# Kernel tuning notes

Measured on AMD Instinct MI355X. Metric: run time of the kernel, lower is better.

The kernel has to match this reference:

```python
import jax, jax.numpy as jnp
import numpy as np

N = 40000
K = 16
NUM_CLASSES = 8
BN_EPS = 1e-5


def _mlp(h, W1, b1, g, bt, m, v, W2, b2):
    # Linear -> ReLU -> BatchNorm1d (eval mode, running stats) -> Linear
    h = jax.nn.relu(h @ W1 + b1)
    h = (h - m) / jnp.sqrt(v + BN_EPS) * g + bt
    return h @ W2 + b2


def _normals(pos, nbr):
    # cross product of first two neighbor offsets, normalized; fallback [0,0,1]
    v1 = pos[nbr[:, 0]] - pos
    v2 = pos[nbr[:, 1]] - pos
    n = jnp.cross(v1, v2)
    nrm = jnp.linalg.norm(n, axis=-1, keepdims=True)
    unit = n / jnp.maximum(nrm, 1e-12)
    up = jnp.array([0.0, 0.0, 1.0], dtype=pos.dtype)
    return jnp.where(nrm > 0, unit, up)


def _pointnet_conv(x, pos, nbr_all, W1, b1, g, bt, m, v, W2, b2):
    # PyG PointNetConv: msg = local_nn(cat[x_j, pos_j - pos_i]); max-aggregate
    xj = x[nbr_all]                        # [N, K+1, F]
    rel = pos[nbr_all] - pos[:, None, :]   # [N, K+1, 3]
    msg = _mlp(jnp.concatenate([xj, rel], axis=-1), W1, b1, g, bt, m, v, W2, b2)
    return msg.max(axis=1)


def setup_inputs():
    key = jax.random.key(0)
    ks = jax.random.split(key, 32)

    def lin_w(k, fi, fo):
        return (jax.random.normal(k, (fi, fo), jnp.float32) / np.sqrt(fi)).astype(jnp.float32)

    def vec(k, d, scale=0.01):
        return scale * jax.random.normal(k, (d,), jnp.float32)

    return {
        "pos": jax.random.normal(ks[0], (N, 3), jnp.float32),
        "neighbor_idx": jax.random.randint(ks[1], (N, K), 0, N),
        # local_features: Linear(9,64), ReLU, BN(64), Linear(64,128)
        "W1": lin_w(ks[2], 9, 64), "b1": vec(ks[3], 64),
        "g1": 1.0 + 0.1 * jax.random.normal(ks[4], (64,), jnp.float32),
        "bt1": vec(ks[5], 64), "m1": vec(ks[6], 64, 0.1),
        "v1": jax.random.uniform(ks[7], (64,), jnp.float32, minval=0.5, maxval=1.5),
        "W2": lin_w(ks[8], 64, 128), "b2": vec(ks[9], 128),
        # roof_features: Linear(131,128), ReLU, BN(128), Linear(128,256)
        "W3": lin_w(ks[10], 131, 128), "b3": vec(ks[11], 128),
        "g2": 1.0 + 0.1 * jax.random.normal(ks[12], (128,), jnp.float32),
        "bt2": vec(ks[13], 128), "m2": vec(ks[14], 128, 0.1),
        "v2": jax.random.uniform(ks[15], (128,), jnp.float32, minval=0.5, maxval=1.5),
        "W4": lin_w(ks[16], 128, 256), "b4": vec(ks[17], 256),
        # classifier: Linear(256, num_classes)
        "Wc": lin_w(ks[18], 256, NUM_CLASSES), "bc": vec(ks[19], NUM_CLASSES),
    }


def reference(pos, neighbor_idx, W1, b1, g1, bt1, m1, v1, W2, b2,
              W3, b3, g2, bt2, m2, v2, W4, b4, Wc, bc):
    x = pos  # data.x is used as both features and coordinates
    normals = _normals(pos, neighbor_idx)
    x = jnp.concatenate([x, normals], axis=1)  # [N, 6]
    # PointNetConv adds self-loops by default
    self_idx = jnp.arange(pos.shape[0], dtype=neighbor_idx.dtype)[:, None]
    nbr_all = jnp.concatenate([neighbor_idx, self_idx], axis=1)  # [N, K+1]
    x = jax.nn.relu(_pointnet_conv(x, pos, nbr_all, W1, b1, g1, bt1, m1, v1, W2, b2))
    x = jax.nn.relu(_pointnet_conv(x, pos, nbr_all, W3, b3, g2, bt2, m2, v2, W4, b4))
    logits = x @ Wc + bc
    return jax.nn.log_softmax(logits, axis=-1)
```

## Files before the change

kernel.cpp:

```cpp
#include <hip/hip_runtime.h>
#include <math.h>

#define NPTS 40000
#define KNBR 16
#define BN_EPS 1e-5f

typedef __attribute__((ext_vector_type(8))) short v8s;
typedef __attribute__((ext_vector_type(4))) float f32x4;

__device__ __forceinline__ unsigned short f2bf(float f) {
    union { float f; unsigned int u; } c; c.f = f;
    unsigned int u = c.u + 0x7fffu + ((c.u >> 16) & 1u);
    return (unsigned short)(u >> 16);
}
__device__ __forceinline__ float bflo(unsigned int u) {
    union { unsigned int u; float f; } c; c.u = u << 16; return c.f;
}
__device__ __forceinline__ float bfhi(unsigned int u) {
    union { unsigned int u; float f; } c; c.u = u & 0xffff0000u; return c.f;
}
__device__ __forceinline__ float bf2f(unsigned short u) {
    union { unsigned int u; float f; } c; c.u = ((unsigned int)u) << 16; return c.f;
}

__global__ __launch_bounds__(256, 4)
void k1_b1(const float* __restrict__ pos, const int* __restrict__ nbr,
           const float* __restrict__ W1, const float* __restrict__ b1,
           unsigned short* __restrict__ B1) {
    int p = blockIdx.x * 4 + (threadIdx.x >> 6);
    int k = threadIdx.x & 63;
    float px = pos[p * 3 + 0], py = pos[p * 3 + 1], pz = pos[p * 3 + 2];
    int n0 = nbr[p * KNBR + 0], n1 = nbr[p * KNBR + 1];
    float ax = pos[n0 * 3 + 0] - px, ay = pos[n0 * 3 + 1] - py, az = pos[n0 * 3 + 2] - pz;
    float bx = pos[n1 * 3 + 0] - px, by = pos[n1 * 3 + 1] - py, bz = pos[n1 * 3 + 2] - pz;
    float cx = ay * bz - az * by;
    float cy = az * bx - ax * bz;
    float cz = ax * by - ay * bx;
    float nrm = sqrtf(cx * cx + cy * cy + cz * cz);
    float inv = 1.0f / fmaxf(nrm, 1e-12f);
    float ux, uy, uz;
    if (nrm > 0.0f) { ux = cx * inv; uy = cy * inv; uz = cz * inv; }
    else            { ux = 0.0f;     uy = 0.0f;     uz = 1.0f;     }
    float acc = b1[k];
    acc = fmaf(px, W1[0 * 64 + k], acc);
    acc = fmaf(py, W1[1 * 64 + k], acc);
    acc = fmaf(pz, W1[2 * 64 + k], acc);
    acc = fmaf(ux, W1[3 * 64 + k], acc);
    acc = fmaf(uy, W1[4 * 64 + k], acc);
    acc = fmaf(uz, W1[5 * 64 + k], acc);
    B1[p * 64 + k] = f2bf(acc);
}

#define PTS2 32
#define NG2 8
__global__ __launch_bounds__(256, 2)
void k2_conv1_mfma(const float* __restrict__ pos, const int* __restrict__ nbr,
                   const unsigned short* __restrict__ B1, const float* __restrict__ W1,
                   const float* __restrict__ g1, const float* __restrict__ bt1,
                   const float* __restrict__ m1, const float* __restrict__ v1,
                   const float* __restrict__ W2, const float* __restrict__ b2,
                   const float* __restrict__ W3, const float* __restrict__ b3,
                   unsigned short* __restrict__ A2) {
    __shared__ __align__(16) unsigned char Tl[2][64 * 128];
    __shared__ __align__(16) unsigned char Hl[32 * 256];
    __shared__ unsigned short Ssb[32 * 128];

    const int tid  = threadIdx.x;
    const int wv   = tid >> 6;
    const int lane = tid & 63;
    const int lgrp = lane >> 4;
    const int lmod = lane & 15;

    v8s Bf2[2][2];
    float b2c[2];
#pragma unroll
    for (int nt = 0; nt < 2; ++nt) {
        const int col = wv * 32 + nt * 16 + lmod;
        b2c[nt] = b2[col];
#pragma unroll
        for (int kt = 0; kt < 2; ++kt)
#pragma unroll
            for (int j = 0; j < 8; ++j)
                Bf2[nt][kt][j] = (short)f2bf(W2[(kt * 32 + lgrp * 8 + j) * 128 + col]);
    }
    const int ch = lane;
    const float w6 = W1[6 * 64 + ch], w7 = W1[7 * 64 + ch], w8 = W1[8 * 64 + ch];
    const float s1 = g1[ch] * rsqrtf(v1[ch] + BN_EPS);
    const float o1 = bt1[ch] - m1[ch] * s1;

    const int base = blockIdx.x * PTS2;

#pragma unroll
    for (int r = 0; r < 8; ++r) {
        const int pl = wv * 8 + r;
        const float bv = bf2f(B1[(size_t)(base + pl) * 64 + ch]);
        const float t = fmaf(fmaxf(bv, 0.f), s1, o1);
        int byte = pl * 128 + ch * 2;
        byte ^= (pl & 7) << 4;
        *(unsigned short*)(Tl[0] + byte) = f2bf(t);
    }
    __syncthreads();
    {
        f32x4 accS[2][2];
#pragma unroll
        for (int hf = 0; hf < 2; ++hf)
#pragma unroll
            for (int nt = 0; nt < 2; ++nt) accS[hf][nt] = f32x4{0.f, 0.f, 0.f, 0.f};
#pragma unroll
        for (int hf = 0; hf < 2; ++hf)
#pragma unroll
            for (int kt = 0; kt < 2; ++kt) {
                const int row = hf * 16 + lmod;
                int b0 = row * 128 + kt * 64 + lgrp * 16;
                b0 ^= (row & 7) << 4;
                const v8s a0 = *(const v8s*)(Tl[0] + b0);
#pragma unroll
                for (int nt = 0; nt < 2; ++nt)
                    accS[hf][nt] = __builtin_amdgcn_mfma_f32_16x16x32_bf16(a0, Bf2[nt][kt], accS[hf][nt], 0, 0, 0);
            }
#pragma unroll
        for (int hf = 0; hf < 2; ++hf)
#pragma unroll
            for (int nt = 0; nt < 2; ++nt)
#pragma unroll
                for (int reg = 0; reg < 4; ++reg)
                    Ssb[(hf * 16 + lgrp * 4 + reg) * 128 + wv * 32 + nt * 16 + lmod] =
                        f2bf(accS[hf][nt][reg]);
    }
    __syncthreads();

    {
        const int i0 = base + wv;
        const float cx = pos[i0 * 3 + 0], cy = pos[i0 * 3 + 1], cz = pos[i0 * 3 + 2];
#pragma unroll
        for (int m = 0; m < 16; ++m) {
            int idx = nbr[i0 * KNBR + m];
            idx = __builtin_amdgcn_readfirstlane(idx);
            const float bv = bf2f(B1[(size_t)idx * 64 + ch]);
            const float rx = pos[idx * 3 + 0] - cx;
            const float ry = pos[idx * 3 + 1] - cy;
            const float rz = pos[idx * 3 + 2] - cz;
            float pre = bv;
            pre = fmaf(rx, w6, pre); pre = fmaf(ry, w7, pre); pre = fmaf(rz, w8, pre);
            const float t = fmaf(fmaxf(pre, 0.f), s1, o1);
            const int row = wv * 16 + m;
            int byte = row * 128 + ch * 2;
            byte ^= (row & 7) << 4;
            *(unsigned short*)(Tl[0] + byte) = f2bf(t);
        }
    }
    __syncthreads();

    unsigned short aN[16];
    int idxN[16];
    float cNx = 0.f, cNy = 0.f, cNz = 0.f;
    for (int g = 0; g < NG2; ++g) {
        const int buf = g & 1;
        if (g < NG2 - 1) {
            const int iN = base + (g + 1) * 4 + wv;
            cNx = pos[iN * 3 + 0]; cNy = pos[iN * 3 + 1]; cNz = pos[iN * 3 + 2];
#pragma unroll
            for (int m = 0; m < 16; ++m) {
                int idx = nbr[iN * KNBR + m];
                idx = __builtin_amdgcn_readfirstlane(idx);
                idxN[m] = idx;
                aN[m] = B1[(size_t)idx * 64 + ch];
            }
        }
#pragma unroll
        for (int rb = 0; rb < 4; ++rb) {
            f32x4 acc[2];
            acc[0] = f32x4{0.f, 0.f, 0.f, 0.f};
            acc[1] = f32x4{0.f, 0.f, 0.f, 0.f};
#pragma unroll
            for (int kt = 0; kt < 2; ++kt) {
                const int row = rb * 16 + lmod;
                int b0 = row * 128 + kt * 64 + lgrp * 16;
                b0 ^= (row & 7) << 4;
                const v8s a0 = *(const v8s*)(Tl[buf] + b0);
#pragma unroll
                for (int nt = 0; nt < 2; ++nt)
                    acc[nt] = __builtin_amdgcn_mfma_f32_16x16x32_bf16(a0, Bf2[nt][kt], acc[nt], 0, 0, 0);
            }
            const int pl = g * 4 + rb;
#pragma unroll
            for (int nt = 0; nt < 2; ++nt) {
                float mv = fmaxf(fmaxf(acc[nt][0], acc[nt][1]),
                                 fmaxf(acc[nt][2], acc[nt][3]));
                mv = fmaxf(mv, __shfl_xor(mv, 16));
                mv = fmaxf(mv, __shfl_xor(mv, 32));
                const float ss = bf2f(Ssb[pl * 128 + wv * 32 + nt * 16 + lmod]);
                const float h = fmaxf(fmaxf(mv, ss) + b2c[nt], 0.f);
                if (lgrp == 0) {
                    int hb = pl * 256 + (wv * 32 + nt * 16 + lmod) * 2;
                    hb ^= (pl & 7) << 4;
                    *(unsigned short*)(Hl + hb) = f2bf(h);
                }
            }
        }
        if (g < NG2 - 1) {
#pragma unroll
            for (int m = 0; m < 16; ++m) {
                const int idx = idxN[m];
                const float rx = pos[idx * 3 + 0] - cNx;
                const float ry = pos[idx * 3 + 1] - cNy;
                const float rz = pos[idx * 3 + 2] - cNz;
                float pre = bf2f(aN[m]);
                pre = fmaf(rx, w6, pre); pre = fmaf(ry, w7, pre); pre = fmaf(rz, w8, pre);
                const float t = fmaf(fmaxf(pre, 0.f), s1, o1);
                const int row = wv * 16 + m;
                int byte = row * 128 + ch * 2;
                byte ^= (row & 7) << 4;
                *(unsigned short*)(Tl[buf ^ 1] + byte) = f2bf(t);
            }
        }
        __syncthreads();
    }

    v8s Wf3[2][4];
    float b3c[2];
#pragma unroll
    for (int nt = 0; nt < 2; ++nt) {
        const int col = wv * 32 + nt * 16 + lmod;
        b3c[nt] = b3[col];
#pragma unroll
        for (int kt = 0; kt < 4; ++kt)
#pragma unroll
            for (int j = 0; j < 8; ++j)
                Wf3[nt][kt][j] = (short)f2bf(W3[(kt * 32 + lgrp * 8 + j) * 128 + col]);
    }
    f32x4 accA[2][2];
#pragma unroll
    for (int mt = 0; mt < 2; ++mt)
#pragma unroll
        for (int nt = 0; nt < 2; ++nt) accA[mt][nt] = f32x4{0.f, 0.f, 0.f, 0.f};
#pragma unroll
    for (int kt = 0; kt < 4; ++kt) {
#pragma unroll
        for (int mt = 0; mt < 2; ++mt) {
            int ba = (mt * 16 + lmod) * 256 + kt * 64 + lgrp * 16;
            ba ^= (lmod & 7) << 4;
            const v8s aH = *(const v8s*)(Hl + ba);
#pragma unroll
            for (int nt = 0; nt < 2; ++nt)
                accA[mt][nt] = __builtin_amdgcn_mfma_f32_16x16x32_bf16(aH, Wf3[nt][kt], accA[mt][nt], 0, 0, 0);
        }
    }
#pragma unroll
    for (int mt = 0; mt < 2; ++mt)
#pragma unroll
        for (int nt = 0; nt < 2; ++nt)
#pragma unroll
            for (int reg = 0; reg < 4; ++reg) {
                const int row = base + mt * 16 + lgrp * 4 + reg;
                const int col = wv * 32 + nt * 16 + lmod;
                A2[(size_t)row * 128 + col] = f2bf(accA[mt][nt][reg] + b3c[nt]);
            }
}

#define PTS4 32
#define NG4 8
__global__ __launch_bounds__(256, 2)
void k4_conv2_mfma(const float* __restrict__ pos, const int* __restrict__ nbr,
                   const unsigned short* __restrict__ A2, const float* __restrict__ W3,
                   const float* __restrict__ g2, const float* __restrict__ bt2,
                   const float* __restrict__ m2, const float* __restrict__ v2,
                   const float* __restrict__ W4, const float* __restrict__ b4,
                   const float* __restrict__ Wc,
                   float* __restrict__ Z) {
    __shared__ __align__(16) unsigned char Tl[2][64 * 256];
    __shared__ unsigned short Ssb[32 * 256];

    const int tid  = threadIdx.x;
    const int wv   = tid >> 6;
    const int lane = tid & 63;
    const int lgrp = lane >> 4;
    const int lmod = lane & 15;

    v8s Bf[4][4];
#pragma unroll
    for (int nt = 0; nt < 4; ++nt) {
        const int col = wv * 64 + nt * 16 + lmod;
#pragma unroll
        for (int kt = 0; kt < 4; ++kt)
#pragma unroll
            for (int j = 0; j < 8; ++j)
                Bf[nt][kt][j] = (short)f2bf(W4[(kt * 32 + lgrp * 8 + j) * 256 + col]);
    }
    float b4c[4];
#pragma unroll
    for (int nt = 0; nt < 4; ++nt) b4c[nt] = b4[wv * 64 + nt * 16 + lmod];
    const int ch0 = lane * 2;
    const float bw0a = W3[128 * 128 + ch0],     bw1a = W3[129 * 128 + ch0],     bw2a = W3[130 * 128 + ch0];
    const float bw0b = W3[128 * 128 + ch0 + 1], bw1b = W3[129 * 128 + ch0 + 1], bw2b = W3[130 * 128 + ch0 + 1];
    const float sa = g2[ch0] * rsqrtf(v2[ch0] + BN_EPS);
    const float oa = bt2[ch0] - m2[ch0] * sa;
    const float sb = g2[ch0 + 1] * rsqrtf(v2[ch0 + 1] + BN_EPS);
    const float ob = bt2[ch0 + 1] - m2[ch0 + 1] * sb;

    const int base = blockIdx.x * PTS4;

#pragma unroll
    for (int r = 0; r < 8; ++r) {
        const int pl = wv * 8 + r;
        const unsigned int a = *(const unsigned int*)&A2[(size_t)(base + pl) * 128 + ch0];
        const float ta = fmaf(fmaxf(bflo(a), 0.f), sa, oa);
        const float tb = fmaf(fmaxf(bfhi(a), 0.f), sb, ob);
        const unsigned int w = (unsigned int)f2bf(ta) | ((unsigned int)f2bf(tb) << 16);
        int byte = pl * 256 + ch0 * 2;
        byte ^= (pl & 7) << 4;
        *(unsigned int*)(Tl[0] + byte) = w;
    }
    __syncthreads();
    {
        f32x4 accS[2][4];
#pragma unroll
        for (int hf = 0; hf < 2; ++hf)
#pragma unroll
            for (int nt = 0; nt < 4; ++nt) accS[hf][nt] = f32x4{0.f, 0.f, 0.f, 0.f};
#pragma unroll
        for (int hf = 0; hf < 2; ++hf)
#pragma unroll
            for (int kt = 0; kt < 4; ++kt) {
                const int row = hf * 16 + lmod;
                int b0 = row * 256 + kt * 64 + lgrp * 16;
                b0 ^= (row & 7) << 4;
                const v8s a0 = *(const v8s*)(Tl[0] + b0);
#pragma unroll
                for (int nt = 0; nt < 4; ++nt)
                    accS[hf][nt] = __builtin_amdgcn_mfma_f32_16x16x32_bf16(a0, Bf[nt][kt], accS[hf][nt], 0, 0, 0);
            }
#pragma unroll
        for (int hf = 0; hf < 2; ++hf)
#pragma unroll
            for (int nt = 0; nt < 4; ++nt)
#pragma unroll
                for (int reg = 0; reg < 4; ++reg)
                    Ssb[(hf * 16 + lgrp * 4 + reg) * 256 + wv * 64 + nt * 16 + lmod] =
                        f2bf(accS[hf][nt][reg]);
    }
    __syncthreads();

    {
        const int i0 = base + wv;
        const float cx = pos[i0 * 3 + 0], cy = pos[i0 * 3 + 1], cz = pos[i0 * 3 + 2];
#pragma unroll
        for (int m = 0; m < 16; ++m) {
            int idx = nbr[i0 * KNBR + m];
            idx = __builtin_amdgcn_readfirstlane(idx);
            const unsigned int a = *(const unsigned int*)&A2[(size_t)idx * 128 + ch0];
            const float rx = pos[idx * 3 + 0] - cx;
            const float ry = pos[idx * 3 + 1] - cy;
            const float rz = pos[idx * 3 + 2] - cz;
            float pa = bflo(a);
            pa = fmaf(rx, bw0a, pa); pa = fmaf(ry, bw1a, pa); pa = fmaf(rz, bw2a, pa);
            float pb = bfhi(a);
            pb = fmaf(rx, bw0b, pb); pb = fmaf(ry, bw1b, pb); pb = fmaf(rz, bw2b, pb);
            const float ta = fmaf(fmaxf(pa, 0.f), sa, oa);
            const float tb = fmaf(fmaxf(pb, 0.f), sb, ob);
            const unsigned int w = (unsigned int)f2bf(ta) | ((unsigned int)f2bf(tb) << 16);
            const int row = wv * 16 + m;
            int byte = row * 256 + ch0 * 2;
            byte ^= (row & 7) << 4;
            *(unsigned int*)(Tl[0] + byte) = w;
        }
    }
    __syncthreads();

    unsigned int aN[16];
    int idxN[16];
    float cNx = 0.f, cNy = 0.f, cNz = 0.f;
    for (int g = 0; g < NG4; ++g) {
        const int buf = g & 1;
        if (g < NG4 - 1) {
            const int iN = base + (g + 1) * 4 + wv;
            cNx = pos[iN * 3 + 0]; cNy = pos[iN * 3 + 1]; cNz = pos[iN * 3 + 2];
#pragma unroll
            for (int m = 0; m < 16; ++m) {
                int idx = nbr[iN * KNBR + m];
                idx = __builtin_amdgcn_readfirstlane(idx);
                idxN[m] = idx;
                aN[m] = *(const unsigned int*)&A2[(size_t)idx * 128 + ch0];
            }
        }
#pragma unroll
        for (int rb = 0; rb < 4; ++rb) {
            f32x4 acc[4];
#pragma unroll
            for (int nt = 0; nt < 4; ++nt) acc[nt] = f32x4{0.f, 0.f, 0.f, 0.f};
#pragma unroll
            for (int kt = 0; kt < 4; ++kt) {
                const int row = rb * 16 + lmod;
                int b0 = row * 256 + kt * 64 + lgrp * 16;
                b0 ^= (row & 7) << 4;
                const v8s a0 = *(const v8s*)(Tl[buf] + b0);
#pragma unroll
                for (int nt = 0; nt < 4; ++nt)
                    acc[nt] = __builtin_amdgcn_mfma_f32_16x16x32_bf16(a0, Bf[nt][kt], acc[nt], 0, 0, 0);
            }
            const int pl = g * 4 + rb;
            float part[8];
#pragma unroll
            for (int c = 0; c < 8; ++c) part[c] = 0.f;
#pragma unroll
            for (int nt = 0; nt < 4; ++nt) {
                float mv = fmaxf(fmaxf(acc[nt][0], acc[nt][1]),
                                 fmaxf(acc[nt][2], acc[nt][3]));
                mv = fmaxf(mv, __shfl_xor(mv, 16));
                mv = fmaxf(mv, __shfl_xor(mv, 32));
                const float ss = bf2f(Ssb[pl * 256 + wv * 64 + nt * 16 + lmod]);
                const float h = fmaxf(fmaxf(mv, ss) + b4c[nt], 0.f);
                const int col = wv * 64 + nt * 16 + lmod;
                const float4 wc0 = *(const float4*)&Wc[col * 8 + 0];
                const float4 wc1 = *(const float4*)&Wc[col * 8 + 4];
                part[0] = fmaf(h, wc0.x, part[0]); part[1] = fmaf(h, wc0.y, part[1]);
                part[2] = fmaf(h, wc0.z, part[2]); part[3] = fmaf(h, wc0.w, part[3]);
                part[4] = fmaf(h, wc1.x, part[4]); part[5] = fmaf(h, wc1.y, part[5]);
                part[6] = fmaf(h, wc1.z, part[6]); part[7] = fmaf(h, wc1.w, part[7]);
            }
#pragma unroll
            for (int c = 0; c < 8; ++c) {
                part[c] += __shfl_xor(part[c], 1);
                part[c] += __shfl_xor(part[c], 2);
                part[c] += __shfl_xor(part[c], 4);
                part[c] += __shfl_xor(part[c], 8);
            }
            if (lane == 0) {
#pragma unroll
                for (int c = 0; c < 8; ++c)
                    Z[(size_t)(base + pl) * 32 + wv * 8 + c] = part[c];
            }
        }
        if (g < NG4 - 1) {
#pragma unroll
            for (int m = 0; m < 16; ++m) {
                const int idx = idxN[m];
                const float rx = pos[idx * 3 + 0] - cNx;
                const float ry = pos[idx * 3 + 1] - cNy;
                const float rz = pos[idx * 3 + 2] - cNz;
                float pa = bflo(aN[m]);
                pa = fmaf(rx, bw0a, pa); pa = fmaf(ry, bw1a, pa); pa = fmaf(rz, bw2a, pa);
                float pb = bfhi(aN[m]);
                pb = fmaf(rx, bw0b, pb); pb = fmaf(ry, bw1b, pb); pb = fmaf(rz, bw2b, pb);
                const float ta = fmaf(fmaxf(pa, 0.f), sa, oa);
                const float tb = fmaf(fmaxf(pb, 0.f), sb, ob);
                const unsigned int w = (unsigned int)f2bf(ta) | ((unsigned int)f2bf(tb) << 16);
                const int row = wv * 16 + m;
                int byte = row * 256 + ch0 * 2;
                byte ^= (row & 7) << 4;
                *(unsigned int*)(Tl[buf ^ 1] + byte) = w;
            }
        }
        __syncthreads();
    }
}

__global__ __launch_bounds__(256, 4)
void k5_softmax(const float* __restrict__ Z, const float* __restrict__ bc,
                float* __restrict__ out) {
    const int i = blockIdx.x * 256 + threadIdx.x;
    if (i >= NPTS) return;
    float z[8];
#pragma unroll
    for (int c = 0; c < 8; ++c) z[c] = bc[c];
#pragma unroll
    for (int w = 0; w < 4; ++w) {
        const float4 a = *(const float4*)&Z[(size_t)i * 32 + w * 8 + 0];
        const float4 b = *(const float4*)&Z[(size_t)i * 32 + w * 8 + 4];
        z[0] += a.x; z[1] += a.y; z[2] += a.z; z[3] += a.w;
        z[4] += b.x; z[5] += b.y; z[6] += b.z; z[7] += b.w;
    }
    float mz = z[0];
#pragma unroll
    for (int c = 1; c < 8; ++c) mz = fmaxf(mz, z[c]);
    float se = 0.f;
#pragma unroll
    for (int c = 0; c < 8; ++c) se += expf(z[c] - mz);
    const float lse = mz + logf(se);
#pragma unroll
    for (int c = 0; c < 8; ++c) out[(size_t)i * 8 + c] = z[c] - lse;
}

extern "C" void kernel_launch(void* const* d_in, const int* in_sizes, int n_in,
                              void* d_out, int out_size, void* d_ws, size_t ws_size,
                              hipStream_t stream) {
    const float* pos = (const float*)d_in[0];
    const int*   nbr = (const int*)d_in[1];
    const float* W1  = (const float*)d_in[2];
    const float* b1  = (const float*)d_in[3];
    const float* g1  = (const float*)d_in[4];
    const float* bt1 = (const float*)d_in[5];
    const float* m1  = (const float*)d_in[6];
    const float* v1  = (const float*)d_in[7];
    const float* W2  = (const float*)d_in[8];
    const float* b2  = (const float*)d_in[9];
    const float* W3  = (const float*)d_in[10];
    const float* b3  = (const float*)d_in[11];
    const float* g2  = (const float*)d_in[12];
    const float* bt2 = (const float*)d_in[13];
    const float* m2  = (const float*)d_in[14];
    const float* v2  = (const float*)d_in[15];
    const float* W4  = (const float*)d_in[16];
    const float* b4  = (const float*)d_in[17];
    const float* Wc  = (const float*)d_in[18];
    const float* bc  = (const float*)d_in[19];
    float* out = (float*)d_out;

    unsigned short* B1 = (unsigned short*)d_ws;
    unsigned short* A2 = B1 + (size_t)NPTS * 64;
    float* Z = (float*)(A2 + (size_t)NPTS * 128);

    k1_b1<<<NPTS / 4, 256, 0, stream>>>(pos, nbr, W1, b1, B1);
    k2_conv1_mfma<<<NPTS / PTS2, 256, 0, stream>>>(pos, nbr, B1, W1, g1, bt1, m1, v1,
                                                   W2, b2, W3, b3, A2);
    k4_conv2_mfma<<<NPTS / PTS4, 256, 0, stream>>>(pos, nbr, A2, W3, g2, bt2, m2, v2,
                                                   W4, b4, Wc, Z);
    k5_softmax<<<(NPTS + 255) / 256, 256, 0, stream>>>(Z, bc, out);
}
```

Baseline: 319.8 us.

## Split conv2 into gather-materialize kernel and streaming MFMA GEMM kernel

Replaces the fused conv2 kernel with two kernels. The first gathers neighbour features, applies the positional term, ReLU and BN, and writes the bf16 rows to a global buffer. The second streams these rows through MFMA with W4, max-reduces and applies the classifier. This decouples the irregular gathers from tensor-core work and removes LDS staging and block barriers. In exchange it round-trips a large intermediate through HBM and may chunk the work into several launches if the workspace is small.

```diff
diff --git a/kernel.cpp b/kernel.cpp
--- a/kernel.cpp
+++ b/kernel.cpp
@@ -7,11 +7,12 @@
 
 typedef __attribute__((ext_vector_type(8))) short v8s;
 typedef __attribute__((ext_vector_type(4))) float f32x4;
-
-__device__ __forceinline__ unsigned short f2bf(float f) {
+typedef unsigned short us;
+
+__device__ __forceinline__ us f2bf(float f) {
     union { float f; unsigned int u; } c; c.f = f;
     unsigned int u = c.u + 0x7fffu + ((c.u >> 16) & 1u);
-    return (unsigned short)(u >> 16);
+    return (us)(u >> 16);
 }
 __device__ __forceinline__ float bflo(unsigned int u) {
     union { unsigned int u; float f; } c; c.u = u << 16; return c.f;
@@ -19,14 +20,14 @@
 __device__ __forceinline__ float bfhi(unsigned int u) {
     union { unsigned int u; float f; } c; c.u = u & 0xffff0000u; return c.f;
 }
-__device__ __forceinline__ float bf2f(unsigned short u) {
+__device__ __forceinline__ float bf2f(us u) {
     union { unsigned int u; float f; } c; c.u = ((unsigned int)u) << 16; return c.f;
 }
 
 __global__ __launch_bounds__(256, 4)
 void k1_b1(const float* __restrict__ pos, const int* __restrict__ nbr,
            const float* __restrict__ W1, const float* __restrict__ b1,
-           unsigned short* __restrict__ B1) {
+           us* __restrict__ B1) {
     int p = blockIdx.x * 4 + (threadIdx.x >> 6);
     int k = threadIdx.x & 63;
     float px = pos[p * 3 + 0], py = pos[p * 3 + 1], pz = pos[p * 3 + 2];
@@ -55,15 +56,15 @@
 #define NG2 8
 __global__ __launch_bounds__(256, 2)
 void k2_conv1_mfma(const float* __restrict__ pos, const int* __restrict__ nbr,
-                   const unsigned short* __restrict__ B1, const float* __restrict__ W1,
+                   const us* __restrict__ B1, const float* __restrict__ W1,
                    const float* __restrict__ g1, const float* __restrict__ bt1,
                    const float* __restrict__ m1, const float* __restrict__ v1,
                    const float* __restrict__ W2, const float* __restrict__ b2,
                    const float* __restrict__ W3, const float* __restrict__ b3,
-                   unsigned short* __restrict__ A2) {
+                   us* __restrict__ A2) {
     __shared__ __align__(16) unsigned char Tl[2][64 * 128];
     __shared__ __align__(16) unsigned char Hl[32 * 256];
-    __shared__ unsigned short Ssb[32 * 128];
+    __shared__ us Ssb[32 * 128];
 
     const int tid  = threadIdx.x;
     const int wv   = tid >> 6;
@@ -97,7 +98,7 @@
         const float t = fmaf(fmaxf(bv, 0.f), s1, o1);
         int byte = pl * 128 + ch * 2;
         byte ^= (pl & 7) << 4;
-        *(unsigned short*)(Tl[0] + byte) = f2bf(t);
+        *(us*)(Tl[0] + byte) = f2bf(t);
     }
     __syncthreads();
     {
@@ -146,12 +147,12 @@
             const int row = wv * 16 + m;
             int byte = row * 128 + ch * 2;
             byte ^= (row & 7) << 4;
-            *(unsigned short*)(Tl[0] + byte) = f2bf(t);
+            *(us*)(Tl[0] + byte) = f2bf(t);
         }
     }
     __syncthreads();
 
-    unsigned short aN[16];
+    us aN[16];
     int idxN[16];
     float cNx = 0.f, cNy = 0.f, cNz = 0.f;
     for (int g = 0; g < NG2; ++g) {
@@ -194,7 +195,7 @@
                 if (lgrp == 0) {
                     int hb = pl * 256 + (wv * 32 + nt * 16 + lmod) * 2;
                     hb ^= (pl & 7) << 4;
-                    *(unsigned short*)(Hl + hb) = f2bf(h);
+                    *(us*)(Hl + hb) = f2bf(h);
                 }
             }
         }
@@ -211,7 +212,7 @@
                 const int row = wv * 16 + m;
                 int byte = row * 128 + ch * 2;
                 byte ^= (row & 7) << 4;
-                *(unsigned short*)(Tl[buf ^ 1] + byte) = f2bf(t);
+                *(us*)(Tl[buf ^ 1] + byte) = f2bf(t);
             }
         }
         __syncthreads();
@@ -258,38 +259,16 @@
             }
 }
 
-#define PTS4 32
-#define NG4 8
-__global__ __launch_bounds__(256, 2)
-void k4_conv2_mfma(const float* __restrict__ pos, const int* __restrict__ nbr,
-                   const unsigned short* __restrict__ A2, const float* __restrict__ W3,
-                   const float* __restrict__ g2, const float* __restrict__ bt2,
-                   const float* __restrict__ m2, const float* __restrict__ v2,
-                   const float* __restrict__ W4, const float* __restrict__ b4,
-                   const float* __restrict__ Wc,
-                   float* __restrict__ Z) {
-    __shared__ __align__(16) unsigned char Tl[2][64 * 256];
-    __shared__ unsigned short Ssb[32 * 256];
-
-    const int tid  = threadIdx.x;
-    const int wv   = tid >> 6;
-    const int lane = tid & 63;
-    const int lgrp = lane >> 4;
-    const int lmod = lane & 15;
-
-    v8s Bf[4][4];
-#pragma unroll
-    for (int nt = 0; nt < 4; ++nt) {
-        const int col = wv * 64 + nt * 16 + lmod;
-#pragma unroll
-        for (int kt = 0; kt < 4; ++kt)
-#pragma unroll
-            for (int j = 0; j < 8; ++j)
-                Bf[nt][kt][j] = (short)f2bf(W4[(kt * 32 + lgrp * 8 + j) * 256 + col]);
-    }
-    float b4c[4];
-#pragma unroll
-    for (int nt = 0; nt < 4; ++nt) b4c[nt] = b4[wv * 64 + nt * 16 + lmod];
+__global__ __launch_bounds__(256, 4)
+void k4a_mat(const float* __restrict__ pos, const int* __restrict__ nbr,
+             const us* __restrict__ A2, const float* __restrict__ W3,
+             const float* __restrict__ g2, const float* __restrict__ bt2,
+             const float* __restrict__ m2, const float* __restrict__ v2,
+             us* __restrict__ T, us* __restrict__ Tself,
+             int c0, int npts) {
+    const int lane = threadIdx.x & 63;
+    const int gw = blockIdx.x * 4 + (threadIdx.x >> 6);
+    const int nw = gridDim.x * 4;
     const int ch0 = lane * 2;
     const float bw0a = W3[128 * 128 + ch0],     bw1a = W3[129 * 128 + ch0],     bw2a = W3[130 * 128 + ch0];
     const float bw0b = W3[128 * 128 + ch0 + 1], bw1b = W3[129 * 128 + ch0 + 1], bw2b = W3[130 * 128 + ch0 + 1];
@@ -298,160 +277,117 @@
     const float sb = g2[ch0 + 1] * rsqrtf(v2[ch0 + 1] + BN_EPS);
     const float ob = bt2[ch0 + 1] - m2[ch0 + 1] * sb;
 
-    const int base = blockIdx.x * PTS4;
-
-#pragma unroll
-    for (int r = 0; r < 8; ++r) {
-        const int pl = wv * 8 + r;
-        const unsigned int a = *(const unsigned int*)&A2[(size_t)(base + pl) * 128 + ch0];
+    const int nrows = npts * 16;
+    for (int row = gw; row < nrows; row += nw) {
+        const int il = row >> 4, j = row & 15;
+        const int i = c0 + il;
+        const int idx = nbr[i * KNBR + j];
+        const unsigned int a = *(const unsigned int*)&A2[(size_t)idx * 128 + ch0];
+        const float rx = pos[idx * 3 + 0] - pos[i * 3 + 0];
+        const float ry = pos[idx * 3 + 1] - pos[i * 3 + 1];
+        const float rz = pos[idx * 3 + 2] - pos[i * 3 + 2];
+        float pa = bflo(a);
+        pa = fmaf(rx, bw0a, pa); pa = fmaf(ry, bw1a, pa); pa = fmaf(rz, bw2a, pa);
+        float pb = bfhi(a);
+        pb = fmaf(rx, bw0b, pb); pb = fmaf(ry, bw1b, pb); pb = fmaf(rz, bw2b, pb);
+        const float ta = fmaf(fmaxf(pa, 0.f), sa, oa);
+        const float tb = fmaf(fmaxf(pb, 0.f), sb, ob);
+        const unsigned int w = (unsigned int)f2bf(ta) | ((unsigned int)f2bf(tb) << 16);
+        *(unsigned int*)((unsigned char*)T + (size_t)row * 256 + ch0 * 2) = w;
+    }
+    for (int p = gw; p < npts; p += nw) {
+        const int i = c0 + p;
+        const unsigned int a = *(const unsigned int*)&A2[(size_t)i * 128 + ch0];
         const float ta = fmaf(fmaxf(bflo(a), 0.f), sa, oa);
         const float tb = fmaf(fmaxf(bfhi(a), 0.f), sb, ob);
         const unsigned int w = (unsigned int)f2bf(ta) | ((unsigned int)f2bf(tb) << 16);
-        int byte = pl * 256 + ch0 * 2;
-        byte ^= (pl & 7) << 4;
-        *(unsigned int*)(Tl[0] + byte) = w;
-    }
-    __syncthreads();
-    {
-        f32x4 accS[2][4];
-#pragma unroll
-        for (int hf = 0; hf < 2; ++hf)
-#pragma unroll
-            for (int nt = 0; nt < 4; ++nt) accS[hf][nt] = f32x4{0.f, 0.f, 0.f, 0.f};
-#pragma unroll
-        for (int hf = 0; hf < 2; ++hf)
-#pragma unroll
-            for (int kt = 0; kt < 4; ++kt) {
-                const int row = hf * 16 + lmod;
-                int b0 = row * 256 + kt * 64 + lgrp * 16;
-                b0 ^= (row & 7) << 4;
-                const v8s a0 = *(const v8s*)(Tl[0] + b0);
-#pragma unroll
-                for (int nt = 0; nt < 4; ++nt)
-                    accS[hf][nt] = __builtin_amdgcn_mfma_f32_16x16x32_bf16(a0, Bf[nt][kt], accS[hf][nt], 0, 0, 0);
-            }
-#pragma unroll
-        for (int hf = 0; hf < 2; ++hf)
+        *(unsigned int*)((unsigned char*)Tself + (size_t)i * 256 + ch0 * 2) = w;
+    }
+}
+
+__global__ __launch_bounds__(256, 2)
+void k4b_gemm(const us* __restrict__ T, const us* __restrict__ Tself,
+              const float* __restrict__ W4, const float* __restrict__ b4,
+              const float* __restrict__ Wc, float* __restrict__ Z,
+              int c0, int npts) {
+    const int tid  = threadIdx.x;
+    const int wv   = tid >> 6;
+    const int lane = tid & 63;
+    const int lgrp = lane >> 4;
+    const int lmod = lane & 15;
+
+    v8s Bf[4][4];
+#pragma unroll
+    for (int nt = 0; nt < 4; ++nt) {
+        const int col = wv * 64 + nt * 16 + lmod;
+#pragma unroll
+        for (int kt = 0; kt < 4; ++kt)
+#pragma unroll
+            for (int j = 0; j < 8; ++j)
+                Bf[nt][kt][j] = (short)f2bf(W4[(kt * 32 + lgrp * 8 + j) * 256 + col]);
+    }
+    float b4c[4];
+#pragma unroll
+    for (int nt = 0; nt < 4; ++nt) b4c[nt] = b4[wv * 64 + nt * 16 + lmod];
+
+    const int plb = blockIdx.x * 16;
+    const unsigned char* Tb = (const unsigned char*)T;
+    const unsigned char* Tsb = (const unsigned char*)Tself;
+
+    f32x4 sacc[4];
+#pragma unroll
+    for (int nt = 0; nt < 4; ++nt) sacc[nt] = f32x4{0.f, 0.f, 0.f, 0.f};
+#pragma unroll
+    for (int kt = 0; kt < 4; ++kt) {
+        const v8s a0 = *(const v8s*)(Tsb + (size_t)(c0 + plb + lmod) * 256 + kt * 64 + lgrp * 16);
+#pragma unroll
+        for (int nt = 0; nt < 4; ++nt)
+            sacc[nt] = __builtin_amdgcn_mfma_f32_16x16x32_bf16(a0, Bf[nt][kt], sacc[nt], 0, 0, 0);
+    }
+
+#pragma unroll
+    for (int r = 0; r < 16; ++r) {
+        f32x4 acc[4];
+#pragma unroll
+        for (int nt = 0; nt < 4; ++nt) acc[nt] = f32x4{0.f, 0.f, 0.f, 0.f};
+#pragma unroll
+        for (int kt = 0; kt < 4; ++kt) {
+            const v8s a0 = *(const v8s*)(Tb + (size_t)((plb + r) * 16 + lmod) * 256 + kt * 64 + lgrp * 16);
 #pragma unroll
             for (int nt = 0; nt < 4; ++nt)
-#pragma unroll
-                for (int reg = 0; reg < 4; ++reg)
-                    Ssb[(hf * 16 + lgrp * 4 + reg) * 256 + wv * 64 + nt * 16 + lmod] =
-                        f2bf(accS[hf][nt][reg]);
-    }
-    __syncthreads();
-
-    {
-        const int i0 = base + wv;
-        const float cx = pos[i0 * 3 + 0], cy = pos[i0 * 3 + 1], cz = pos[i0 * 3 + 2];
-#pragma unroll
-        for (int m = 0; m < 16; ++m) {
-            int idx = nbr[i0 * KNBR + m];
-            idx = __builtin_amdgcn_readfirstlane(idx);
-            const unsigned int a = *(const unsigned int*)&A2[(size_t)idx * 128 + ch0];
-            const float rx = pos[idx * 3 + 0] - cx;
-            const float ry = pos[idx * 3 + 1] - cy;
-            const float rz = pos[idx * 3 + 2] - cz;
-            float pa = bflo(a);
-            pa = fmaf(rx, bw0a, pa); pa = fmaf(ry, bw1a, pa); pa = fmaf(rz, bw2a, pa);
-            float pb = bfhi(a);
-            pb = fmaf(rx, bw0b, pb); pb = fmaf(ry, bw1b, pb); pb = fmaf(rz, bw2b, pb);
-            const float ta = fmaf(fmaxf(pa, 0.f), sa, oa);
-            const float tb = fmaf(fmaxf(pb, 0.f), sb, ob);
-            const unsigned int w = (unsigned int)f2bf(ta) | ((unsigned int)f2bf(tb) << 16);
-            const int row = wv * 16 + m;
-            int byte = row * 256 + ch0 * 2;
-            byte ^= (row & 7) << 4;
-            *(unsigned int*)(Tl[0] + byte) = w;
-        }
-    }
-    __syncthreads();
-
-    unsigned int aN[16];
-    int idxN[16];
-    float cNx = 0.f, cNy = 0.f, cNz = 0.f;
-    for (int g = 0; g < NG4; ++g) {
-        const int buf = g & 1;
-        if (g < NG4 - 1) {
-            const int iN = base + (g + 1) * 4 + wv;
-            cNx = pos[iN * 3 + 0]; cNy = pos[iN * 3 + 1]; cNz = pos[iN * 3 + 2];
-#pragma unroll
-            for (int m = 0; m < 16; ++m) {
-                int idx = nbr[iN * KNBR + m];
-                idx = __builtin_amdgcn_readfirstlane(idx);
-                idxN[m] = idx;
-                aN[m] = *(const unsigned int*)&A2[(size_t)idx * 128 + ch0];
-            }
-        }
-#pragma unroll
-        for (int rb = 0; rb < 4; ++rb) {
-            f32x4 acc[4];
-#pragma unroll
-            for (int nt = 0; nt < 4; ++nt) acc[nt] = f32x4{0.f, 0.f, 0.f, 0.f};
-#pragma unroll
-            for (int kt = 0; kt < 4; ++kt) {
-                const int row = rb * 16 + lmod;
-                int b0 = row * 256 + kt * 64 + lgrp * 16;
-                b0 ^= (row & 7) << 4;
-                const v8s a0 = *(const v8s*)(Tl[buf] + b0);
-#pragma unroll
-                for (int nt = 0; nt < 4; ++nt)
-                    acc[nt] = __builtin_amdgcn_mfma_f32_16x16x32_bf16(a0, Bf[nt][kt], acc[nt], 0, 0, 0);
-            }
-            const int pl = g * 4 + rb;
-            float part[8];
-#pragma unroll
-            for (int c = 0; c < 8; ++c) part[c] = 0.f;
-#pragma unroll
-            for (int nt = 0; nt < 4; ++nt) {
-                float mv = fmaxf(fmaxf(acc[nt][0], acc[nt][1]),
-                                 fmaxf(acc[nt][2], acc[nt][3]));
-                mv = fmaxf(mv, __shfl_xor(mv, 16));
-                mv = fmaxf(mv, __shfl_xor(mv, 32));
-                const float ss = bf2f(Ssb[pl * 256 + wv * 64 + nt * 16 + lmod]);
-                const float h = fmaxf(fmaxf(mv, ss) + b4c[nt], 0.f);
-                const int col = wv * 64 + nt * 16 + lmod;
-                const float4 wc0 = *(const float4*)&Wc[col * 8 + 0];
-                const float4 wc1 = *(const float4*)&Wc[col * 8 + 4];
-                part[0] = fmaf(h, wc0.x, part[0]); part[1] = fmaf(h, wc0.y, part[1]);
-                part[2] = fmaf(h, wc0.z, part[2]); part[3] = fmaf(h, wc0.w, part[3]);
-                part[4] = fmaf(h, wc1.x, part[4]); part[5] = fmaf(h, wc1.y, part[5]);
-                part[6] = fmaf(h, wc1.z, part[6]); part[7] = fmaf(h, wc1.w, part[7]);
-            }
-#pragma unroll
-            for (int c = 0; c < 8; ++c) {
-                part[c] += __shfl_xor(part[c], 1);
-                part[c] += __shfl_xor(part[c], 2);
-                part[c] += __shfl_xor(part[c], 4);
-                part[c] += __shfl_xor(part[c], 8);
-            }
-            if (lane == 0) {
-#pragma unroll
-                for (int c = 0; c < 8; ++c)
-                    Z[(size_t)(base + pl) * 32 + wv * 8 + c] = part[c];
-            }
-        }
-        if (g < NG4 - 1) {
-#pragma unroll
-            for (int m = 0; m < 16; ++m) {
-                const int idx = idxN[m];
-                const float rx = pos[idx * 3 + 0] - cNx;
-                const float ry = pos[idx * 3 + 1] - cNy;
-                const float rz = pos[idx * 3 + 2] - cNz;
-                float pa = bflo(aN[m]);
-                pa = fmaf(rx, bw0a, pa); pa = fmaf(ry, bw1a, pa); pa = fmaf(rz, bw2a, pa);
-                float pb = bfhi(aN[m]);
-                pb = fmaf(rx, bw0b, pb); pb = fmaf(ry, bw1b, pb); pb = fmaf(rz, bw2b, pb);
-                const float ta = fmaf(fmaxf(pa, 0.f), sa, oa);
-                const float tb = fmaf(fmaxf(pb, 0.f), sb, ob);
-                const unsigned int w = (unsigned int)f2bf(ta) | ((unsigned int)f2bf(tb) << 16);
-                const int row = wv * 16 + m;
-                int byte = row * 256 + ch0 * 2;
-                byte ^= (row & 7) << 4;
-                *(unsigned int*)(Tl[buf ^ 1] + byte) = w;
-            }
-        }
-        __syncthreads();
+                acc[nt] = __builtin_amdgcn_mfma_f32_16x16x32_bf16(a0, Bf[nt][kt], acc[nt], 0, 0, 0);
+        }
+        float part[8];
+#pragma unroll
+        for (int c = 0; c < 8; ++c) part[c] = 0.f;
+#pragma unroll
+        for (int nt = 0; nt < 4; ++nt) {
+            float mv = fmaxf(fmaxf(acc[nt][0], acc[nt][1]),
+                             fmaxf(acc[nt][2], acc[nt][3]));
+            mv = fmaxf(mv, __shfl_xor(mv, 16));
+            mv = fmaxf(mv, __shfl_xor(mv, 32));
+            const float ss = __shfl(sacc[nt][r & 3], (r >> 2) * 16 + lmod);
+            const float h = fmaxf(fmaxf(mv, ss) + b4c[nt], 0.f);
+            const int col = wv * 64 + nt * 16 + lmod;
+            const float4 wc0 = *(const float4*)&Wc[col * 8 + 0];
+            const float4 wc1 = *(const float4*)&Wc[col * 8 + 4];
+            part[0] = fmaf(h, wc0.x, part[0]); part[1] = fmaf(h, wc0.y, part[1]);
+            part[2] = fmaf(h, wc0.z, part[2]); part[3] = fmaf(h, wc0.w, part[3]);
+            part[4] = fmaf(h, wc1.x, part[4]); part[5] = fmaf(h, wc1.y, part[5]);
+            part[6] = fmaf(h, wc1.z, part[6]); part[7] = fmaf(h, wc1.w, part[7]);
+        }
+#pragma unroll
+        for (int c = 0; c < 8; ++c) {
+            part[c] += __shfl_xor(part[c], 1);
+            part[c] += __shfl_xor(part[c], 2);
+            part[c] += __shfl_xor(part[c], 4);
+            part[c] += __shfl_xor(part[c], 8);
+        }
+        if (lane == 0) {
+#pragma unroll
+            for (int c = 0; c < 8; ++c)
+                Z[(size_t)(c0 + plb + r) * 32 + wv * 8 + c] = part[c];
+        }
     }
 }
 
@@ -506,14 +442,27 @@
     const float* bc  = (const float*)d_in[19];
     float* out = (float*)d_out;
 
-    unsigned short* B1 = (unsigned short*)d_ws;
-    unsigned short* A2 = B1 + (size_t)NPTS * 64;
-    float* Z = (float*)(A2 + (size_t)NPTS * 128);
+    us* B1    = (us*)d_ws;
+    us* A2    = B1 + (size_t)NPTS * 64;
+    us* Tself = A2 + (size_t)NPTS * 128;
+    float* Z  = (float*)(Tself + (size_t)NPTS * 128);
+    us* T     = (us*)(Z + (size_t)NPTS * 32);
+
+    const size_t fixed = (size_t)NPTS * (64 + 128 + 128) * 2 + (size_t)NPTS * 32 * 4;
+    int chunk = 40000;
+    if (fixed + (size_t)chunk * 16 * 256 > ws_size) chunk = 20000;
+    if (fixed + (size_t)chunk * 16 * 256 > ws_size) chunk = 8000;
+    if (fixed + (size_t)chunk * 16 * 256 > ws_size) chunk = 4000;
+    const int nch = NPTS / chunk;
 
     k1_b1<<<NPTS / 4, 256, 0, stream>>>(pos, nbr, W1, b1, B1);
     k2_conv1_mfma<<<NPTS / PTS2, 256, 0, stream>>>(pos, nbr, B1, W1, g1, bt1, m1, v1,
                                                    W2, b2, W3, b3, A2);
-    k4_conv2_mfma<<<NPTS / PTS4, 256, 0, stream>>>(pos, nbr, A2, W3, g2, bt2, m2, v2,
-                                                   W4, b4, Wc, Z);
+    for (int c = 0; c < nch; ++c) {
+        k4a_mat<<<512, 256, 0, stream>>>(pos, nbr, A2, W3, g2, bt2, m2, v2,
+                                         T, Tself, c * chunk, chunk);
+        k4b_gemm<<<chunk / 16, 256, 0, stream>>>(T, Tself, W4, b4, Wc, Z,
+                                                 c * chunk, chunk);
+    }
     k5_softmax<<<(NPTS + 255) / 256, 256, 0, stream>>>(Z, bc, out);
 }
```

Measured after the change: 455.1 us. +42.3%, slower.

## Restructure conv2 kernel to process one point per step with two-deep prefetch

Applied to the files above, without the earlier changes.

The conv2 kernel's main loop now handles one point per iteration instead of four. Each wave gathers 4 of the 16 neighbours for that point, and the neighbour features and positions for the point two steps ahead are prefetched into registers. The shared tile buffers shrink from 64 rows to 16, and the classifier weights are cached in registers instead of being reloaded from global memory on every step. The aim is to cut per-thread register and LDS pressure and hide gather latency better, at the cost of 32 block-wide barriers per block instead of 8 and four times as many small MFMA/reduction rounds.

```diff
diff --git a/kernel.cpp b/kernel.cpp
--- a/kernel.cpp
+++ b/kernel.cpp
@@ -7,11 +7,12 @@
 
 typedef __attribute__((ext_vector_type(8))) short v8s;
 typedef __attribute__((ext_vector_type(4))) float f32x4;
-
-__device__ __forceinline__ unsigned short f2bf(float f) {
+typedef unsigned short us;
+
+__device__ __forceinline__ us f2bf(float f) {
     union { float f; unsigned int u; } c; c.f = f;
     unsigned int u = c.u + 0x7fffu + ((c.u >> 16) & 1u);
-    return (unsigned short)(u >> 16);
+    return (us)(u >> 16);
 }
 __device__ __forceinline__ float bflo(unsigned int u) {
     union { unsigned int u; float f; } c; c.u = u << 16; return c.f;
@@ -19,14 +20,14 @@
 __device__ __forceinline__ float bfhi(unsigned int u) {
     union { unsigned int u; float f; } c; c.u = u & 0xffff0000u; return c.f;
 }
-__device__ __forceinline__ float bf2f(unsigned short u) {
+__device__ __forceinline__ float bf2f(us u) {
     union { unsigned int u; float f; } c; c.u = ((unsigned int)u) << 16; return c.f;
 }
 
 __global__ __launch_bounds__(256, 4)
 void k1_b1(const float* __restrict__ pos, const int* __restrict__ nbr,
            const float* __restrict__ W1, const float* __restrict__ b1,
-           unsigned short* __restrict__ B1) {
+           us* __restrict__ B1) {
     int p = blockIdx.x * 4 + (threadIdx.x >> 6);
     int k = threadIdx.x & 63;
     float px = pos[p * 3 + 0], py = pos[p * 3 + 1], pz = pos[p * 3 + 2];
@@ -55,15 +56,15 @@
 #define NG2 8
 __global__ __launch_bounds__(256, 2)
 void k2_conv1_mfma(const float* __restrict__ pos, const int* __restrict__ nbr,
-                   const unsigned short* __restrict__ B1, const float* __restrict__ W1,
+                   const us* __restrict__ B1, const float* __restrict__ W1,
                    const float* __restrict__ g1, const float* __restrict__ bt1,
                    const float* __restrict__ m1, const float* __restrict__ v1,
                    const float* __restrict__ W2, const float* __restrict__ b2,
                    const float* __restrict__ W3, const float* __restrict__ b3,
-                   unsigned short* __restrict__ A2) {
+                   us* __restrict__ A2) {
     __shared__ __align__(16) unsigned char Tl[2][64 * 128];
     __shared__ __align__(16) unsigned char Hl[32 * 256];
-    __shared__ unsigned short Ssb[32 * 128];
+    __shared__ us Ssb[32 * 128];
 
     const int tid  = threadIdx.x;
     const int wv   = tid >> 6;
@@ -97,7 +98,7 @@
         const float t = fmaf(fmaxf(bv, 0.f), s1, o1);
         int byte = pl * 128 + ch * 2;
         byte ^= (pl & 7) << 4;
-        *(unsigned short*)(Tl[0] + byte) = f2bf(t);
+        *(us*)(Tl[0] + byte) = f2bf(t);
     }
     __syncthreads();
     {
@@ -146,12 +147,12 @@
             const int row = wv * 16 + m;
             int byte = row * 128 + ch * 2;
             byte ^= (row & 7) << 4;
-            *(unsigned short*)(Tl[0] + byte) = f2bf(t);
+            *(us*)(Tl[0] + byte) = f2bf(t);
         }
     }
     __syncthreads();
 
-    unsigned short aN[16];
+    us aN[16];
     int idxN[16];
     float cNx = 0.f, cNy = 0.f, cNz = 0.f;
     for (int g = 0; g < NG2; ++g) {
@@ -194,7 +195,7 @@
                 if (lgrp == 0) {
                     int hb = pl * 256 + (wv * 32 + nt * 16 + lmod) * 2;
                     hb ^= (pl & 7) << 4;
-                    *(unsigned short*)(Hl + hb) = f2bf(h);
+                    *(us*)(Hl + hb) = f2bf(h);
                 }
             }
         }
@@ -211,7 +212,7 @@
                 const int row = wv * 16 + m;
                 int byte = row * 128 + ch * 2;
                 byte ^= (row & 7) << 4;
-                *(unsigned short*)(Tl[buf ^ 1] + byte) = f2bf(t);
+                *(us*)(Tl[buf ^ 1] + byte) = f2bf(t);
             }
         }
         __syncthreads();
@@ -259,17 +260,16 @@
 }
 
 #define PTS4 32
-#define NG4 8
 __global__ __launch_bounds__(256, 2)
 void k4_conv2_mfma(const float* __restrict__ pos, const int* __restrict__ nbr,
-                   const unsigned short* __restrict__ A2, const float* __restrict__ W3,
+                   const us* __restrict__ A2, const float* __restrict__ W3,
                    const float* __restrict__ g2, const float* __restrict__ bt2,
                    const float* __restrict__ m2, const float* __restrict__ v2,
                    const float* __restrict__ W4, const float* __restrict__ b4,
                    const float* __restrict__ Wc,
                    float* __restrict__ Z) {
-    __shared__ __align__(16) unsigned char Tl[2][64 * 256];
-    __shared__ unsigned short Ssb[32 * 256];
+    __shared__ __align__(16) unsigned char Tl[2][16 * 256];
+    __shared__ us Ssb[32 * 256];
 
     const int tid  = threadIdx.x;
     const int wv   = tid >> 6;
@@ -287,9 +287,14 @@
             for (int j = 0; j < 8; ++j)
                 Bf[nt][kt][j] = (short)f2bf(W4[(kt * 32 + lgrp * 8 + j) * 256 + col]);
     }
-    float b4c[4];
-#pragma unroll
-    for (int nt = 0; nt < 4; ++nt) b4c[nt] = b4[wv * 64 + nt * 16 + lmod];
+    float wcls[4][8]; float b4c[4];
+#pragma unroll
+    for (int nt = 0; nt < 4; ++nt) {
+        const int col = wv * 64 + nt * 16 + lmod;
+        b4c[nt] = b4[col];
+#pragma unroll
+        for (int c = 0; c < 8; ++c) wcls[nt][c] = Wc[col * 8 + c];
+    }
     const int ch0 = lane * 2;
     const float bw0a = W3[128 * 128 + ch0],     bw1a = W3[129 * 128 + ch0],     bw2a = W3[130 * 128 + ch0];
     const float bw0b = W3[128 * 128 + ch0 + 1], bw1b = W3[129 * 128 + ch0 + 1], bw2b = W3[130 * 128 + ch0 + 1];
@@ -307,9 +312,10 @@
         const float ta = fmaf(fmaxf(bflo(a), 0.f), sa, oa);
         const float tb = fmaf(fmaxf(bfhi(a), 0.f), sb, ob);
         const unsigned int w = (unsigned int)f2bf(ta) | ((unsigned int)f2bf(tb) << 16);
-        int byte = pl * 256 + ch0 * 2;
-        byte ^= (pl & 7) << 4;
-        *(unsigned int*)(Tl[0] + byte) = w;
+        const int row = pl & 15;
+        int byte = row * 256 + ch0 * 2;
+        byte ^= (row & 7) << 4;
+        *(unsigned int*)(Tl[pl >> 4] + byte) = w;
     }
     __syncthreads();
     {
@@ -322,10 +328,9 @@
         for (int hf = 0; hf < 2; ++hf)
 #pragma unroll
             for (int kt = 0; kt < 4; ++kt) {
-                const int row = hf * 16 + lmod;
-                int b0 = row * 256 + kt * 64 + lgrp * 16;
-                b0 ^= (row & 7) << 4;
-                const v8s a0 = *(const v8s*)(Tl[0] + b0);
+                int b0 = lmod * 256 + kt * 64 + lgrp * 16;
+                b0 ^= (lmod & 7) << 4;
+                const v8s a0 = *(const v8s*)(Tl[hf] + b0);
 #pragma unroll
                 for (int nt = 0; nt < 4; ++nt)
                     accS[hf][nt] = __builtin_amdgcn_mfma_f32_16x16x32_bf16(a0, Bf[nt][kt], accS[hf][nt], 0, 0, 0);
@@ -342,12 +347,12 @@
     __syncthreads();
 
     {
-        const int i0 = base + wv;
-        const float cx = pos[i0 * 3 + 0], cy = pos[i0 * 3 + 1], cz = pos[i0 * 3 + 2];
-#pragma unroll
-        for (int m = 0; m < 16; ++m) {
-            int idx = nbr[i0 * KNBR + m];
-            idx = __builtin_amdgcn_readfirstlane(idx);
+        const int i = base;
+        const float cx = pos[i * 3 + 0], cy = pos[i * 3 + 1], cz = pos[i * 3 + 2];
+#pragma unroll
+        for (int it = 0; it < 4; ++it) {
+            const int m = it * 4 + wv;
+            const int idx = nbr[i * KNBR + m];
             const unsigned int a = *(const unsigned int*)&A2[(size_t)idx * 128 + ch0];
             const float rx = pos[idx * 3 + 0] - cx;
             const float ry = pos[idx * 3 + 1] - cy;
@@ -359,99 +364,102 @@
             const float ta = fmaf(fmaxf(pa, 0.f), sa, oa);
             const float tb = fmaf(fmaxf(pb, 0.f), sb, ob);
             const unsigned int w = (unsigned int)f2bf(ta) | ((unsigned int)f2bf(tb) << 16);
-            const int row = wv * 16 + m;
-            int byte = row * 256 + ch0 * 2;
-            byte ^= (row & 7) << 4;
+            int byte = m * 256 + ch0 * 2;
+            byte ^= (m & 7) << 4;
             *(unsigned int*)(Tl[0] + byte) = w;
         }
     }
+    unsigned int aCur[4], aNxt[4];
+    float pCx[4], pCy[4], pCz[4], pNx[4], pNy[4], pNz[4];
+#pragma unroll
+    for (int it = 0; it < 4; ++it) { aCur[it] = 0u; aNxt[it] = 0u; pCx[it]=pCy[it]=pCz[it]=pNx[it]=pNy[it]=pNz[it]=0.f; }
+    {
+        const int in_ = base + 1;
+#pragma unroll
+        for (int it = 0; it < 4; ++it) {
+            const int m = it * 4 + wv;
+            const int idx = nbr[in_ * KNBR + m];
+            aCur[it] = *(const unsigned int*)&A2[(size_t)idx * 128 + ch0];
+            pCx[it] = pos[idx * 3 + 0]; pCy[it] = pos[idx * 3 + 1]; pCz[it] = pos[idx * 3 + 2];
+        }
+    }
     __syncthreads();
 
-    unsigned int aN[16];
-    int idxN[16];
-    float cNx = 0.f, cNy = 0.f, cNz = 0.f;
-    for (int g = 0; g < NG4; ++g) {
-        const int buf = g & 1;
-        if (g < NG4 - 1) {
-            const int iN = base + (g + 1) * 4 + wv;
-            cNx = pos[iN * 3 + 0]; cNy = pos[iN * 3 + 1]; cNz = pos[iN * 3 + 2];
-#pragma unroll
-            for (int m = 0; m < 16; ++m) {
-                int idx = nbr[iN * KNBR + m];
-                idx = __builtin_amdgcn_readfirstlane(idx);
-                idxN[m] = idx;
-                aN[m] = *(const unsigned int*)&A2[(size_t)idx * 128 + ch0];
-            }
-        }
-#pragma unroll
-        for (int rb = 0; rb < 4; ++rb) {
-            f32x4 acc[4];
-#pragma unroll
-            for (int nt = 0; nt < 4; ++nt) acc[nt] = f32x4{0.f, 0.f, 0.f, 0.f};
-#pragma unroll
-            for (int kt = 0; kt < 4; ++kt) {
-                const int row = rb * 16 + lmod;
-                int b0 = row * 256 + kt * 64 + lgrp * 16;
-                b0 ^= (row & 7) << 4;
-                const v8s a0 = *(const v8s*)(Tl[buf] + b0);
-#pragma unroll
-                for (int nt = 0; nt < 4; ++nt)
-                    acc[nt] = __builtin_amdgcn_mfma_f32_16x16x32_bf16(a0, Bf[nt][kt], acc[nt], 0, 0, 0);
-            }
-            const int pl = g * 4 + rb;
-            float part[8];
-#pragma unroll
-            for (int c = 0; c < 8; ++c) part[c] = 0.f;
-#pragma unroll
-            for (int nt = 0; nt < 4; ++nt) {
-                float mv = fmaxf(fmaxf(acc[nt][0], acc[nt][1]),
-                                 fmaxf(acc[nt][2], acc[nt][3]));
-                mv = fmaxf(mv, __shfl_xor(mv, 16));
-                mv = fmaxf(mv, __shfl_xor(mv, 32));
-                const float ss = bf2f(Ssb[pl * 256 + wv * 64 + nt * 16 + lmod]);
-                const float h = fmaxf(fmaxf(mv, ss) + b4c[nt], 0.f);
-                const int col = wv * 64 + nt * 16 + lmod;
-                const float4 wc0 = *(const float4*)&Wc[col * 8 + 0];
-                const float4 wc1 = *(const float4*)&Wc[col * 8 + 4];
-                part[0] = fmaf(h, wc0.x, part[0]); part[1] = fmaf(h, wc0.y, part[1]);
-                part[2] = fmaf(h, wc0.z, part[2]); part[3] = fmaf(h, wc0.w, part[3]);
-                part[4] = fmaf(h, wc1.x, part[4]); part[5] = fmaf(h, wc1.y, part[5]);
-                part[6] = fmaf(h, wc1.z, part[6]); part[7] = fmaf(h, wc1.w, part[7]);
-            }
-#pragma unroll
-            for (int c = 0; c < 8; ++c) {
-                part[c] += __shfl_xor(part[c], 1);
-                part[c] += __shfl_xor(part[c], 2);
-                part[c] += __shfl_xor(part[c], 4);
-                part[c] += __shfl_xor(part[c], 8);
-            }
-            if (lane == 0) {
-#pragma unroll
-                for (int c = 0; c < 8; ++c)
-                    Z[(size_t)(base + pl) * 32 + wv * 8 + c] = part[c];
-            }
-        }
-        if (g < NG4 - 1) {
-#pragma unroll
-            for (int m = 0; m < 16; ++m) {
-                const int idx = idxN[m];
-                const float rx = pos[idx * 3 + 0] - cNx;
-                const float ry = pos[idx * 3 + 1] - cNy;
-                const float rz = pos[idx * 3 + 2] - cNz;
-                float pa = bflo(aN[m]);
+    for (int p = 0; p < PTS4; ++p) {
+        const int buf = p & 1;
+        if (p < PTS4 - 2) {
+            const int in2 = base + p + 2;
+#pragma unroll
+            for (int it = 0; it < 4; ++it) {
+                const int m = it * 4 + wv;
+                const int idx = nbr[in2 * KNBR + m];
+                aNxt[it] = *(const unsigned int*)&A2[(size_t)idx * 128 + ch0];
+                pNx[it] = pos[idx * 3 + 0]; pNy[it] = pos[idx * 3 + 1]; pNz[it] = pos[idx * 3 + 2];
+            }
+        }
+        f32x4 acc0[4];
+#pragma unroll
+        for (int nt = 0; nt < 4; ++nt) acc0[nt] = f32x4{0.f, 0.f, 0.f, 0.f};
+#pragma unroll
+        for (int kt = 0; kt < 4; ++kt) {
+            int b0 = lmod * 256 + kt * 64 + lgrp * 16;
+            b0 ^= (lmod & 7) << 4;
+            const v8s a0 = *(const v8s*)(Tl[buf] + b0);
+#pragma unroll
+            for (int nt = 0; nt < 4; ++nt)
+                acc0[nt] = __builtin_amdgcn_mfma_f32_16x16x32_bf16(a0, Bf[nt][kt], acc0[nt], 0, 0, 0);
+        }
+        float part[8];
+#pragma unroll
+        for (int c = 0; c < 8; ++c) part[c] = 0.f;
+#pragma unroll
+        for (int nt = 0; nt < 4; ++nt) {
+            float mv = fmaxf(fmaxf(acc0[nt][0], acc0[nt][1]),
+                             fmaxf(acc0[nt][2], acc0[nt][3]));
+            mv = fmaxf(mv, __shfl_xor(mv, 16));
+            mv = fmaxf(mv, __shfl_xor(mv, 32));
+            const float ss = bf2f(Ssb[p * 256 + wv * 64 + nt * 16 + lmod]);
+            const float h = fmaxf(fmaxf(mv, ss) + b4c[nt], 0.f);
+#pragma unroll
+            for (int c = 0; c < 8; ++c) part[c] = fmaf(h, wcls[nt][c], part[c]);
+        }
+#pragma unroll
+        for (int c = 0; c < 8; ++c) {
+            part[c] += __shfl_xor(part[c], 1);
+            part[c] += __shfl_xor(part[c], 2);
+            part[c] += __shfl_xor(part[c], 4);
+            part[c] += __shfl_xor(part[c], 8);
+        }
+        if (lane == 0) {
+#pragma unroll
+            for (int c = 0; c < 8; ++c)
+                Z[(size_t)(base + p) * 32 + wv * 8 + c] = part[c];
+        }
+        if (p < PTS4 - 1) {
+            const int in_ = base + p + 1;
+            const float ccx = pos[in_ * 3 + 0], ccy = pos[in_ * 3 + 1], ccz = pos[in_ * 3 + 2];
+#pragma unroll
+            for (int it = 0; it < 4; ++it) {
+                const int m = it * 4 + wv;
+                const float rx = pCx[it] - ccx, ry = pCy[it] - ccy, rz = pCz[it] - ccz;
+                float pa = bflo(aCur[it]);
                 pa = fmaf(rx, bw0a, pa); pa = fmaf(ry, bw1a, pa); pa = fmaf(rz, bw2a, pa);
-                float pb = bfhi(aN[m]);
+                float pb = bfhi(aCur[it]);
                 pb = fmaf(rx, bw0b, pb); pb = fmaf(ry, bw1b, pb); pb = fmaf(rz, bw2b, pb);
                 const float ta = fmaf(fmaxf(pa, 0.f), sa, oa);
                 const float tb = fmaf(fmaxf(pb, 0.f), sb, ob);
                 const unsigned int w = (unsigned int)f2bf(ta) | ((unsigned int)f2bf(tb) << 16);
-                const int row = wv * 16 + m;
-                int byte = row * 256 + ch0 * 2;
-                byte ^= (row & 7) << 4;
+                int byte = m * 256 + ch0 * 2;
+                byte ^= (m & 7) << 4;
                 *(unsigned int*)(Tl[buf ^ 1] + byte) = w;
             }
         }
         __syncthreads();
+#pragma unroll
+        for (int it = 0; it < 4; ++it) {
+            aCur[it] = aNxt[it];
+            pCx[it] = pNx[it]; pCy[it] = pNy[it]; pCz[it] = pNz[it];
+        }
     }
 }
 
@@ -506,8 +514,8 @@
     const float* bc  = (const float*)d_in[19];
     float* out = (float*)d_out;
 
-    unsigned short* B1 = (unsigned short*)d_ws;
-    unsigned short* A2 = B1 + (size_t)NPTS * 64;
+    us* B1   = (us*)d_ws;
+    us* A2   = B1 + (size_t)NPTS * 64;
     float* Z = (float*)(A2 + (size_t)NPTS * 128);
 
     k1_b1<<<NPTS / 4, 256, 0, stream>>>(pos, nbr, W1, b1, B1);
```

Measured after the change: 319.3 us. No clear change (-0.1%).
